# Kernel tuning notes

Measured on AMD Instinct MI355X. Metric: run time of the kernel, lower is better.

The kernel has to match this reference:

```python
import jax, jax.numpy as jnp
import numpy as np

DIM = 1024
NUM_HEADS = 8  # only used for the scale; heads are never actually split
SCALE = float((DIM // NUM_HEADS) ** 0.5)


def _attn(x, wq, wk, wv):
    # Single-head full-dim attention, faithful to the source (no head split).
    Q = x @ wq.T  # [B,S,D]
    K = x @ wk.T
    V = x @ wv.T
    scores = jnp.einsum('bqd,bkd->bqk', Q, K) / SCALE  # [B,S,S]
    attn = jax.nn.softmax(scores, axis=-1)
    return jnp.einsum('bqk,bkd->bqd', attn, V)


def setup_inputs() -> dict:
    key = jax.random.key(0)
    ks = jax.random.split(key, 9)
    B, S, D = 4, 2048, DIM
    w = lambda k: jax.random.normal(k, (D, D), dtype=jnp.float32) * 0.02
    return {
        'x': jax.random.normal(ks[0], (B, S, D), dtype=jnp.float32),
        'wq1': w(ks[1]), 'wk1': w(ks[2]), 'wv1': w(ks[3]),
        'fc1_w': w(ks[4]),
        'wq2': w(ks[5]), 'wk2': w(ks[6]), 'wv2': w(ks[7]),
        'fc2_w': w(ks[8]),
    }


def reference(x, wq1, wk1, wv1, fc1_w, wq2, wk2, wv2, fc2_w):
    h = _attn(x, wq1, wk1, wv1)
    h = jax.nn.silu(h)
    h = h @ fc1_w.T
    h = _attn(h, wq2, wk2, wv2)
    h = jax.nn.silu(h)
    h = h @ fc2_w.T
    return jax.nn.softmax(h, axis=-1)
```

## Files before the change

kernel.cpp:

```cpp
#include <hip/hip_runtime.h>
#include <math.h>


typedef __attribute__((ext_vector_type(8))) int i32x8;
typedef __attribute__((ext_vector_type(4))) int i32x4;
typedef __attribute__((ext_vector_type(4))) float f32x4;
typedef unsigned char u8;
typedef unsigned int u32;

#define EPI_F32 0
#define EPI_F8 1
#define EPI_QKV 2
#define EPI_SILU_F8 3

__device__ __forceinline__ void gload_lds16(const void* g, void* l) {
    __builtin_amdgcn_global_load_lds(
        (const __attribute__((address_space(1))) void*)g,
        (__attribute__((address_space(3))) void*)l, 16, 0, 0);
}

__device__ __forceinline__ u8 cvt_f8(float v) {
    return (u8)(__builtin_amdgcn_cvt_pk_fp8_f32(v, v, 0, false) & 0xFF);
}

template <int EPI>
__global__ __launch_bounds__(256) void gemm_fp8(
    const u8* __restrict__ A, const u8* __restrict__ B,
    void* __restrict__ C0, void* __restrict__ C1, void* __restrict__ C2,
    int K, int ldA, int ldB, int ldC,
    long long bsA, long long bsB, long long bsC, float alpha, float beta)
{
    __shared__ u8 sA[128 * 128];
    __shared__ u8 sB[128 * 128];

    const int tid = threadIdx.x;
    const int wave = tid >> 6, lane = tid & 63;
    const int wm = wave >> 1, wn = wave & 1;
    const int m0 = blockIdx.y * 128, n0 = blockIdx.x * 128;
    const long long z = blockIdx.z;

    const u8* pA = A + z * bsA;
    const u8* pB = B + z * bsB;

    int blkid[4], rs[4], cs16[4];
#pragma unroll
    for (int i = 0; i < 4; i++) {
        blkid[i] = wave * 256 + i * 64 + lane;
        rs[i] = blkid[i] >> 3;
        cs16[i] = ((blkid[i] & 7) ^ (rs[i] & 7)) * 16;
    }

    f32x4 acc[4][4] = {};
    const int fr = lane & 15, fc2 = (lane >> 4) * 2;

    for (int k0 = 0; k0 < K; k0 += 128) {
#pragma unroll
        for (int i = 0; i < 4; i++) {
            gload_lds16(pA + (long long)(m0 + rs[i]) * ldA + k0 + cs16[i],
                        sA + blkid[i] * 16);
            gload_lds16(pB + (long long)(n0 + rs[i]) * ldB + k0 + cs16[i],
                        sB + blkid[i] * 16);
        }
        __syncthreads();

        i32x8 a[4], b[4];
#pragma unroll
        for (int i = 0; i < 4; i++) {
            const int row = wm * 64 + i * 16 + fr;
            const int sw = row & 7;
            i32x4 lo = *(const i32x4*)(sA + row * 128 + ((fc2 + 0) ^ sw) * 16);
            i32x4 hi = *(const i32x4*)(sA + row * 128 + ((fc2 + 1) ^ sw) * 16);
            a[i] = __builtin_shufflevector(lo, hi, 0, 1, 2, 3, 4, 5, 6, 7);
        }
#pragma unroll
        for (int j = 0; j < 4; j++) {
            const int row = wn * 64 + j * 16 + fr;
            const int sw = row & 7;
            i32x4 lo = *(const i32x4*)(sB + row * 128 + ((fc2 + 0) ^ sw) * 16);
            i32x4 hi = *(const i32x4*)(sB + row * 128 + ((fc2 + 1) ^ sw) * 16);
            b[j] = __builtin_shufflevector(lo, hi, 0, 1, 2, 3, 4, 5, 6, 7);
        }
#pragma unroll
        for (int i = 0; i < 4; i++)
#pragma unroll
            for (int j = 0; j < 4; j++)
                acc[i][j] = __builtin_amdgcn_mfma_scale_f32_16x16x128_f8f6f4(
                    a[i], b[j], acc[i][j], 0 , 0 ,
                    0, 0x7F7F7F7F, 0, 0x7F7F7F7F);
        __syncthreads();
    }

    const int col = lane & 15;
    const int rbase = (lane >> 4) * 4;
#pragma unroll
    for (int i = 0; i < 4; i++) {
#pragma unroll
        for (int j = 0; j < 4; j++) {
            const int mloc = m0 + wm * 64 + i * 16 + rbase;
            const int nloc = n0 + wn * 64 + j * 16 + col;
            float v[4];
#pragma unroll
            for (int r = 0; r < 4; r++) v[r] = acc[i][j][r] * alpha;

            if (EPI == EPI_F32) {
                float* C = (float*)C0 + z * bsC;
#pragma unroll
                for (int r = 0; r < 4; r++)
                    C[(long long)(mloc + r) * ldC + nloc] = v[r];
            } else if (EPI == EPI_F8) {
                u8* C = (u8*)C0 + z * bsC;
#pragma unroll
                for (int r = 0; r < 4; r++)
                    C[(long long)(mloc + r) * ldC + nloc] = cvt_f8(v[r]);
            } else if (EPI == EPI_SILU_F8) {
                u8* C = (u8*)C0 + z * bsC;
#pragma unroll
                for (int r = 0; r < 4; r++) {
                    float s = v[r] / (1.f + __expf(-v[r]));
                    C[(long long)(mloc + r) * ldC + nloc] = cvt_f8(s * beta);
                }
            } else {
                const int seg = nloc >> 10;
                const int nn = nloc & 1023;
                if (seg == 2) {
                    const int bb = mloc >> 11, mm = mloc & 2047;
                    int p01 = __builtin_amdgcn_cvt_pk_fp8_f32(v[0], v[1], 0, false);
                    int p23 = __builtin_amdgcn_cvt_pk_fp8_f32(v[2], v[3], 0, false);
                    u32 pk = (u32)(p01 & 0xFFFF) | ((u32)p23 << 16);
                    *(u32*)((u8*)C2 + (long long)bb * (1024LL * 2048) +
                            (long long)nn * 2048 + mm) = pk;
                } else {
                    u8* C = seg ? (u8*)C1 : (u8*)C0;
#pragma unroll
                    for (int r = 0; r < 4; r++)
                        C[(long long)(mloc + r) * 1024 + nn] = cvt_f8(v[r]);
                }
            }
        }
    }
}

__global__ __launch_bounds__(256) void convert_fp8(
    const float* __restrict__ in, u8* __restrict__ o, long long n, float scale)
{
    long long i = ((long long)blockIdx.x * 256 + threadIdx.x) * 4;
    if (i >= n) return;
    float4 v = *(const float4*)(in + i);
    int p01 = __builtin_amdgcn_cvt_pk_fp8_f32(v.x * scale, v.y * scale, 0, false);
    int p23 = __builtin_amdgcn_cvt_pk_fp8_f32(v.z * scale, v.w * scale, 0, false);
    *(u32*)(o + i) = (u32)(p01 & 0xFFFF) | ((u32)p23 << 16);
}

__global__ __launch_bounds__(256) void softmax_f8_2048(float* __restrict__ sc)
{
    float* p = sc + (long long)blockIdx.x * 2048;
    const int tid = threadIdx.x;
    const int lane = tid & 63, wv = tid >> 6;
    __shared__ float redm[4], reds[4];

    float4 v0 = *(const float4*)(p + tid * 8);
    float4 v1 = *(const float4*)(p + tid * 8 + 4);
    float vals[8] = {v0.x, v0.y, v0.z, v0.w, v1.x, v1.y, v1.z, v1.w};

    float m = -INFINITY;
#pragma unroll
    for (int i = 0; i < 8; i++) m = fmaxf(m, vals[i]);
#pragma unroll
    for (int off = 32; off; off >>= 1) m = fmaxf(m, __shfl_xor(m, off));
    if (lane == 0) redm[wv] = m;
    __syncthreads();
    m = fmaxf(fmaxf(redm[0], redm[1]), fmaxf(redm[2], redm[3]));

    float s = 0.f;
#pragma unroll
    for (int i = 0; i < 8; i++) {
        vals[i] = __expf(vals[i] - m);
        s += vals[i];
    }
#pragma unroll
    for (int off = 32; off; off >>= 1) s += __shfl_xor(s, off);
    if (lane == 0) reds[wv] = s;
    __syncthreads();
    s = reds[0] + reds[1] + reds[2] + reds[3];

    const float inv = 256.0f / s;
    int b01 = __builtin_amdgcn_cvt_pk_fp8_f32(vals[0] * inv, vals[1] * inv, 0, false);
    int b23 = __builtin_amdgcn_cvt_pk_fp8_f32(vals[2] * inv, vals[3] * inv, 0, false);
    int b45 = __builtin_amdgcn_cvt_pk_fp8_f32(vals[4] * inv, vals[5] * inv, 0, false);
    int b67 = __builtin_amdgcn_cvt_pk_fp8_f32(vals[6] * inv, vals[7] * inv, 0, false);
    uint2 w2;
    w2.x = (u32)(b01 & 0xFFFF) | ((u32)b23 << 16);
    w2.y = (u32)(b45 & 0xFFFF) | ((u32)b67 << 16);
    *(uint2*)((u8*)p + tid * 8) = w2;
}

__global__ __launch_bounds__(256) void softmax_1024(
    const float* __restrict__ in, float* __restrict__ out)
{
    const float* p = in + (long long)blockIdx.x * 1024;
    float* o = out + (long long)blockIdx.x * 1024;
    const int tid = threadIdx.x;
    const int lane = tid & 63, wv = tid >> 6;
    __shared__ float redm[4], reds[4];

    float4 v = *(const float4*)(p + tid * 4);
    float vals[4] = {v.x, v.y, v.z, v.w};

    float m = -INFINITY;
#pragma unroll
    for (int i = 0; i < 4; i++) m = fmaxf(m, vals[i]);
#pragma unroll
    for (int off = 32; off; off >>= 1) m = fmaxf(m, __shfl_xor(m, off));
    if (lane == 0) redm[wv] = m;
    __syncthreads();
    m = fmaxf(fmaxf(redm[0], redm[1]), fmaxf(redm[2], redm[3]));

    float s = 0.f;
#pragma unroll
    for (int i = 0; i < 4; i++) {
        vals[i] = __expf(vals[i] - m);
        s += vals[i];
    }
#pragma unroll
    for (int off = 32; off; off >>= 1) s += __shfl_xor(s, off);
    if (lane == 0) reds[wv] = s;
    __syncthreads();
    s = reds[0] + reds[1] + reds[2] + reds[3];
    const float inv = 1.0f / s;
    float4 ov;
    ov.x = vals[0] * inv; ov.y = vals[1] * inv;
    ov.z = vals[2] * inv; ov.w = vals[3] * inv;
    *(float4*)(o + tid * 4) = ov;
}

extern "C" void kernel_launch(void* const* d_in, const int* in_sizes, int n_in,
                              void* d_out, int out_size, void* d_ws, size_t ws_size,
                              hipStream_t stream)
{
    const float* x = (const float*)d_in[0];
    const float* wt[8] = {(const float*)d_in[1], (const float*)d_in[2],
                          (const float*)d_in[3], (const float*)d_in[4],
                          (const float*)d_in[5], (const float*)d_in[6],
                          (const float*)d_in[7], (const float*)d_in[8]};
    float* out = (float*)d_out;

    constexpr int Bt = 4, S = 2048, D = 1024;
    constexpr int M = Bt * S;
    const long long MD = (long long)M * D;
    const long long DD = (long long)D * D;
    const long long SD = (long long)S * D;
    const long long SSf = (long long)Bt * S * S;

    u8* Af = (u8*)d_ws;
    u8* Wf = Af + MD;
    u8* Qf = Wf + 8 * DD;
    u8* Kf = Qf + MD;
    u8* VT = Kf + MD;
    float* SC = (float*)(VT + MD);
    u8* Hs = (u8*)(SC + SSf);

    const dim3 blk(256);

    const float SOFT = 0.08838834764831845f;
    const float a_qkv[2] = {8.f / 2048.f, 1024.f / 65536.f};
    const float a_qk[2]  = {SOFT / 64.f, SOFT / 1048576.f};
    const float a_pv[2]  = {1.f / 2048.f, 1.f / 262144.f};
    const float b_pv[2]  = {256.f, 65536.f};
    const float a_fc[2]  = {256.f / 65536.f, 1.f / (65536.f * 256.f)};

    convert_fp8<<<dim3((int)(MD / 1024)), blk, 0, stream>>>(x, Af, MD, 8.f);
    for (int i = 0; i < 8; i++)
        convert_fp8<<<dim3((int)(DD / 1024)), blk, 0, stream>>>(
            wt[i], Wf + i * DD, DD, 256.f);

    const dim3 gqkv(3 * D / 128, M / 128, 1);
    const dim3 gw(D / 128, M / 128, 1);
    const dim3 gqk(S / 128, S / 128, Bt);
    const dim3 gpv(D / 128, S / 128, Bt);

    const u8* Pf = (const u8*)SC;

    for (int layer = 0; layer < 2; layer++) {
        const u8* wqkv = Wf + (long long)(layer * 4) * DD;
        const u8* fc   = Wf + (long long)(layer * 4 + 3) * DD;

        gemm_fp8<EPI_QKV><<<gqkv, blk, 0, stream>>>(
            Af, wqkv, Qf, Kf, VT, D, D, D, D, 0, 0, 0, a_qkv[layer], 0.f);
        gemm_fp8<EPI_F32><<<gqk, blk, 0, stream>>>(
            Qf, Kf, SC, nullptr, nullptr, D, D, D, S, SD, SD,
            (long long)S * S, a_qk[layer], 0.f);
        softmax_f8_2048<<<dim3(Bt * S), blk, 0, stream>>>(SC);
        gemm_fp8<EPI_SILU_F8><<<gpv, blk, 0, stream>>>(
            Pf, VT, Hs, nullptr, nullptr, S, 4 * S , S, D,
            (long long)S * S * 4 , (long long)D * S,
            SD, a_pv[layer], b_pv[layer]);
        if (layer == 0) {
            gemm_fp8<EPI_F8><<<gw, blk, 0, stream>>>(
                Hs, fc, Af, nullptr, nullptr, D, D, D, D, 0, 0, 0,
                a_fc[0], 0.f);
        } else {
            gemm_fp8<EPI_F32><<<gw, blk, 0, stream>>>(
                Hs, fc, SC, nullptr, nullptr, D, D, D, D, 0, 0, 0,
                a_fc[1], 0.f);
        }
    }

    softmax_1024<<<dim3(M), blk, 0, stream>>>(SC, out);
}
```

Measured before the change: 382.8 us.

## Fuse softmax exp and row-sum into QK GEMM epilogue, normalize in PV

Result: faster. 347.8 us (-9.1%).

```diff
diff --git a/kernel.cpp b/kernel.cpp
--- a/kernel.cpp
+++ b/kernel.cpp
@@ -11,7 +11,8 @@
 #define EPI_F32 0
 #define EPI_F8 1
 #define EPI_QKV 2
-#define EPI_SILU_F8 3
+#define EPI_EXP 3
+#define EPI_PV 4
 
 __device__ __forceinline__ void gload_lds16(const void* g, void* l) {
     __builtin_amdgcn_global_load_lds(
@@ -42,12 +43,12 @@
     const u8* pA = A + z * bsA;
     const u8* pB = B + z * bsB;
 
-    int blkid[4], rs[4], cs16[4];
+    int blkid[4], rs_[4], cs16[4];
 #pragma unroll
     for (int i = 0; i < 4; i++) {
         blkid[i] = wave * 256 + i * 64 + lane;
-        rs[i] = blkid[i] >> 3;
-        cs16[i] = ((blkid[i] & 7) ^ (rs[i] & 7)) * 16;
+        rs_[i] = blkid[i] >> 3;
+        cs16[i] = ((blkid[i] & 7) ^ (rs_[i] & 7)) * 16;
     }
 
     f32x4 acc[4][4] = {};
@@ -56,9 +57,9 @@
     for (int k0 = 0; k0 < K; k0 += 128) {
 #pragma unroll
         for (int i = 0; i < 4; i++) {
-            gload_lds16(pA + (long long)(m0 + rs[i]) * ldA + k0 + cs16[i],
+            gload_lds16(pA + (long long)(m0 + rs_[i]) * ldA + k0 + cs16[i],
                         sA + blkid[i] * 16);
-            gload_lds16(pB + (long long)(n0 + rs[i]) * ldB + k0 + cs16[i],
+            gload_lds16(pB + (long long)(n0 + rs_[i]) * ldB + k0 + cs16[i],
                         sB + blkid[i] * 16);
         }
         __syncthreads();
@@ -92,36 +93,74 @@
 
     const int col = lane & 15;
     const int rbase = (lane >> 4) * 4;
+
+    if (EPI == EPI_EXP) {
+        u8* P = (u8*)C0 + z * bsC;
+        float* rsum = (float*)C1 + z * 2048;
+#pragma unroll
+        for (int i = 0; i < 4; i++) {
+            const int mloc = m0 + wm * 64 + i * 16 + rbase;
+            float rowp[4] = {0.f, 0.f, 0.f, 0.f};
+#pragma unroll
+            for (int j = 0; j < 4; j++) {
+                const int nloc = n0 + wn * 64 + j * 16 + col;
+#pragma unroll
+                for (int r = 0; r < 4; r++) {
+                    float e = __expf(acc[i][j][r] * alpha);
+                    rowp[r] += e;
+                    P[(long long)(mloc + r) * ldC + nloc] = cvt_f8(e * 0.0625f);
+                }
+            }
+#pragma unroll
+            for (int r = 0; r < 4; r++) {
+                float t = rowp[r];
+                t += __shfl_xor(t, 1);
+                t += __shfl_xor(t, 2);
+                t += __shfl_xor(t, 4);
+                t += __shfl_xor(t, 8);
+                if ((lane & 15) == 0) atomicAdd(&rsum[mloc + r], t);
+            }
+        }
+        return;
+    }
+
 #pragma unroll
     for (int i = 0; i < 4; i++) {
+        const int mloc = m0 + wm * 64 + i * 16 + rbase;
+        float inv[4];
+        if (EPI == EPI_PV) {
+            const float* rsum = (const float*)C1 + z * 2048;
+#pragma unroll
+            for (int r = 0; r < 4; r++) inv[r] = alpha / rsum[mloc + r];
+        }
 #pragma unroll
         for (int j = 0; j < 4; j++) {
-            const int mloc = m0 + wm * 64 + i * 16 + rbase;
             const int nloc = n0 + wn * 64 + j * 16 + col;
-            float v[4];
-#pragma unroll
-            for (int r = 0; r < 4; r++) v[r] = acc[i][j][r] * alpha;
-
             if (EPI == EPI_F32) {
                 float* C = (float*)C0 + z * bsC;
 #pragma unroll
                 for (int r = 0; r < 4; r++)
-                    C[(long long)(mloc + r) * ldC + nloc] = v[r];
+                    C[(long long)(mloc + r) * ldC + nloc] = acc[i][j][r] * alpha;
             } else if (EPI == EPI_F8) {
                 u8* C = (u8*)C0 + z * bsC;
 #pragma unroll
                 for (int r = 0; r < 4; r++)
-                    C[(long long)(mloc + r) * ldC + nloc] = cvt_f8(v[r]);
-            } else if (EPI == EPI_SILU_F8) {
+                    C[(long long)(mloc + r) * ldC + nloc] =
+                        cvt_f8(acc[i][j][r] * alpha);
+            } else if (EPI == EPI_PV) {
                 u8* C = (u8*)C0 + z * bsC;
 #pragma unroll
                 for (int r = 0; r < 4; r++) {
-                    float s = v[r] / (1.f + __expf(-v[r]));
-                    C[(long long)(mloc + r) * ldC + nloc] = cvt_f8(s * beta);
+                    float v = acc[i][j][r] * inv[r];
+                    v = v / (1.f + __expf(-v));
+                    C[(long long)(mloc + r) * ldC + nloc] = cvt_f8(v * beta);
                 }
             } else {
                 const int seg = nloc >> 10;
                 const int nn = nloc & 1023;
+                float v[4];
+#pragma unroll
+                for (int r = 0; r < 4; r++) v[r] = acc[i][j][r] * alpha;
                 if (seg == 2) {
                     const int bb = mloc >> 11, mm = mloc & 2047;
                     int p01 = __builtin_amdgcn_cvt_pk_fp8_f32(v[0], v[1], 0, false);
@@ -151,47 +190,19 @@
     *(u32*)(o + i) = (u32)(p01 & 0xFFFF) | ((u32)p23 << 16);
 }
 
-__global__ __launch_bounds__(256) void softmax_f8_2048(float* __restrict__ sc)
-{
-    float* p = sc + (long long)blockIdx.x * 2048;
-    const int tid = threadIdx.x;
-    const int lane = tid & 63, wv = tid >> 6;
-    __shared__ float redm[4], reds[4];
-
-    float4 v0 = *(const float4*)(p + tid * 8);
-    float4 v1 = *(const float4*)(p + tid * 8 + 4);
-    float vals[8] = {v0.x, v0.y, v0.z, v0.w, v1.x, v1.y, v1.z, v1.w};
-
-    float m = -INFINITY;
-#pragma unroll
-    for (int i = 0; i < 8; i++) m = fmaxf(m, vals[i]);
-#pragma unroll
-    for (int off = 32; off; off >>= 1) m = fmaxf(m, __shfl_xor(m, off));
-    if (lane == 0) redm[wv] = m;
-    __syncthreads();
-    m = fmaxf(fmaxf(redm[0], redm[1]), fmaxf(redm[2], redm[3]));
-
-    float s = 0.f;
-#pragma unroll
-    for (int i = 0; i < 8; i++) {
-        vals[i] = __expf(vals[i] - m);
-        s += vals[i];
-    }
-#pragma unroll
-    for (int off = 32; off; off >>= 1) s += __shfl_xor(s, off);
-    if (lane == 0) reds[wv] = s;
-    __syncthreads();
-    s = reds[0] + reds[1] + reds[2] + reds[3];
-
-    const float inv = 256.0f / s;
-    int b01 = __builtin_amdgcn_cvt_pk_fp8_f32(vals[0] * inv, vals[1] * inv, 0, false);
-    int b23 = __builtin_amdgcn_cvt_pk_fp8_f32(vals[2] * inv, vals[3] * inv, 0, false);
-    int b45 = __builtin_amdgcn_cvt_pk_fp8_f32(vals[4] * inv, vals[5] * inv, 0, false);
-    int b67 = __builtin_amdgcn_cvt_pk_fp8_f32(vals[6] * inv, vals[7] * inv, 0, false);
-    uint2 w2;
-    w2.x = (u32)(b01 & 0xFFFF) | ((u32)b23 << 16);
-    w2.y = (u32)(b45 & 0xFFFF) | ((u32)b67 << 16);
-    *(uint2*)((u8*)p + tid * 8) = w2;
+__global__ __launch_bounds__(256) void convert_w8(
+    const float* w0, const float* w1, const float* w2, const float* w3,
+    const float* w4, const float* w5, const float* w6, const float* w7,
+    u8* __restrict__ o)
+{
+    const float* ws[8] = {w0, w1, w2, w3, w4, w5, w6, w7};
+    const float* src = ws[blockIdx.y];
+    long long i = ((long long)blockIdx.x * 256 + threadIdx.x) * 4;
+    float4 v = *(const float4*)(src + i);
+    int p01 = __builtin_amdgcn_cvt_pk_fp8_f32(v.x * 256.f, v.y * 256.f, 0, false);
+    int p23 = __builtin_amdgcn_cvt_pk_fp8_f32(v.z * 256.f, v.w * 256.f, 0, false);
+    *(u32*)(o + (long long)blockIdx.y * 1024 * 1024 + i) =
+        (u32)(p01 & 0xFFFF) | ((u32)p23 << 16);
 }
 
 __global__ __launch_bounds__(256) void softmax_1024(
@@ -238,10 +249,6 @@
                               hipStream_t stream)
 {
     const float* x = (const float*)d_in[0];
-    const float* wt[8] = {(const float*)d_in[1], (const float*)d_in[2],
-                          (const float*)d_in[3], (const float*)d_in[4],
-                          (const float*)d_in[5], (const float*)d_in[6],
-                          (const float*)d_in[7], (const float*)d_in[8]};
     float* out = (float*)d_out;
 
     constexpr int Bt = 4, S = 2048, D = 1024;
@@ -249,51 +256,51 @@
     const long long MD = (long long)M * D;
     const long long DD = (long long)D * D;
     const long long SD = (long long)S * D;
-    const long long SSf = (long long)Bt * S * S;
+    const long long SS = (long long)S * S;
 
     u8* Af = (u8*)d_ws;
     u8* Wf = Af + MD;
     u8* Qf = Wf + 8 * DD;
     u8* Kf = Qf + MD;
     u8* VT = Kf + MD;
-    float* SC = (float*)(VT + MD);
-    u8* Hs = (u8*)(SC + SSf);
+    u8* Pf = VT + MD;
+    u8* Hs = Pf + (long long)Bt * SS;
+    float* SC = (float*)(Hs + MD);
+    float* rsum = SC + MD;
 
     const dim3 blk(256);
 
     const float SOFT = 0.08838834764831845f;
     const float a_qkv[2] = {8.f / 2048.f, 1024.f / 65536.f};
     const float a_qk[2]  = {SOFT / 64.f, SOFT / 1048576.f};
-    const float a_pv[2]  = {1.f / 2048.f, 1.f / 262144.f};
+    const float a_pv[2]  = {2.0f, 1.f / 64.f};
     const float b_pv[2]  = {256.f, 65536.f};
-    const float a_fc[2]  = {256.f / 65536.f, 1.f / (65536.f * 256.f)};
+    const float a_fc[2]  = {256.f / 65536.f, 1.f / 16777216.f};
 
     convert_fp8<<<dim3((int)(MD / 1024)), blk, 0, stream>>>(x, Af, MD, 8.f);
-    for (int i = 0; i < 8; i++)
-        convert_fp8<<<dim3((int)(DD / 1024)), blk, 0, stream>>>(
-            wt[i], Wf + i * DD, DD, 256.f);
+    convert_w8<<<dim3((int)(DD / 1024), 8), blk, 0, stream>>>(
+        (const float*)d_in[1], (const float*)d_in[2], (const float*)d_in[3],
+        (const float*)d_in[4], (const float*)d_in[5], (const float*)d_in[6],
+        (const float*)d_in[7], (const float*)d_in[8], Wf);
 
     const dim3 gqkv(3 * D / 128, M / 128, 1);
     const dim3 gw(D / 128, M / 128, 1);
     const dim3 gqk(S / 128, S / 128, Bt);
     const dim3 gpv(D / 128, S / 128, Bt);
 
-    const u8* Pf = (const u8*)SC;
-
     for (int layer = 0; layer < 2; layer++) {
         const u8* wqkv = Wf + (long long)(layer * 4) * DD;
         const u8* fc   = Wf + (long long)(layer * 4 + 3) * DD;
 
         gemm_fp8<EPI_QKV><<<gqkv, blk, 0, stream>>>(
             Af, wqkv, Qf, Kf, VT, D, D, D, D, 0, 0, 0, a_qkv[layer], 0.f);
-        gemm_fp8<EPI_F32><<<gqk, blk, 0, stream>>>(
-            Qf, Kf, SC, nullptr, nullptr, D, D, D, S, SD, SD,
-            (long long)S * S, a_qk[layer], 0.f);
-        softmax_f8_2048<<<dim3(Bt * S), blk, 0, stream>>>(SC);
-        gemm_fp8<EPI_SILU_F8><<<gpv, blk, 0, stream>>>(
-            Pf, VT, Hs, nullptr, nullptr, S, 4 * S , S, D,
-            (long long)S * S * 4 , (long long)D * S,
-            SD, a_pv[layer], b_pv[layer]);
+        hipMemsetAsync(rsum, 0, (size_t)M * sizeof(float), stream);
+        gemm_fp8<EPI_EXP><<<gqk, blk, 0, stream>>>(
+            Qf, Kf, Pf, rsum, nullptr, D, D, D, S, SD, SD, SS,
+            a_qk[layer], 0.f);
+        gemm_fp8<EPI_PV><<<gpv, blk, 0, stream>>>(
+            Pf, VT, Hs, rsum, nullptr, S, S, S, D, SS, (long long)D * S, SD,
+            a_pv[layer], b_pv[layer]);
         if (layer == 0) {
             gemm_fp8<EPI_F8><<<gw, blk, 0, stream>>>(
                 Hs, fc, Af, nullptr, nullptr, D, D, D, D, 0, 0, 0,
```
